# Optimization experiments

Hardware: AMD Instinct MI355X
Metric: run time of the kernel (lower is better)

Reference implementation:

```python
import jax, jax.numpy as jnp
import numpy as np

D_MODEL = 1024
H = 16
D_K = D_MODEL // H
D_FF = 4096
EPS = 1e-6
NEG = -1e9


def setup_inputs() -> dict:
    key = jax.random.key(0)
    ks = jax.random.split(key, 8)
    B, S = 2, 2048
    src = jax.random.normal(ks[0], (B, S, D_MODEL), dtype=jnp.float32)
    src_mask = jnp.ones((B, 1, 1, S), dtype=jnp.int32)
    sc = 1.0 / np.sqrt(D_MODEL)
    wq = jax.random.normal(ks[1], (D_MODEL, D_MODEL), jnp.float32) * sc
    wk = jax.random.normal(ks[2], (D_MODEL, D_MODEL), jnp.float32) * sc
    wv = jax.random.normal(ks[3], (D_MODEL, D_MODEL), jnp.float32) * sc
    wo = jax.random.normal(ks[4], (D_MODEL, D_MODEL), jnp.float32) * sc
    w1 = jax.random.normal(ks[5], (D_FF, D_MODEL), jnp.float32) * sc
    b1 = jnp.zeros((D_FF,), jnp.float32)
    w2 = jax.random.normal(ks[6], (D_MODEL, D_FF), jnp.float32) * (1.0 / np.sqrt(D_FF))
    b2 = jnp.zeros((D_MODEL,), jnp.float32)
    a1 = jnp.ones((1,), jnp.float32)
    be1 = jnp.zeros((1,), jnp.float32)
    a2 = jnp.ones((1,), jnp.float32)
    be2 = jnp.zeros((1,), jnp.float32)
    return dict(src=src, src_mask=src_mask, wq=wq, wk=wk, wv=wv, wo=wo,
                w1=w1, b1=b1, w2=w2, b2=b2, a1=a1, be1=be1, a2=a2, be2=be2)


def layer_norm(x, alpha, bias):
    # torch: mean + unbiased std (ddof=1), eps added to std
    mean = jnp.mean(x, axis=-1, keepdims=True)
    std = jnp.sqrt(jnp.var(x, axis=-1, keepdims=True, ddof=1))
    return alpha * (x - mean) / (std + EPS) + bias


def mha(x, mask, wq, wk, wv, wo):
    B, S, _ = x.shape
    def split(t):  # [B,S,D] -> [B,H,S,D_K]
        return t.reshape(B, S, H, D_K).transpose(0, 2, 1, 3)
    q = split(x @ wq.T)
    k = split(x @ wk.T)
    v = split(x @ wv.T)
    scores = jnp.einsum('bhqd,bhkd->bhqk', q, k) / np.sqrt(D_K)
    scores = jnp.where(mask == 0, NEG, scores)
    attn = jax.nn.softmax(scores, axis=-1)
    out = jnp.einsum('bhqk,bhkd->bhqd', attn, v)
    out = out.transpose(0, 2, 1, 3).reshape(B, S, D_MODEL)
    return out @ wo.T


def reference(src, src_mask, wq, wk, wv, wo, w1, b1, w2, b2, a1, be1, a2, be2):
    x = layer_norm(src, a1, be1)
    src = src + mha(x, src_mask, wq, wk, wv, wo)
    x = layer_norm(src, a2, be2)
    ff = jax.nn.relu(x @ w1.T + b1) @ w2.T + b2
    return src + ff
```

## Files before the change

kernel.cpp:

```cpp
#include <hip/hip_runtime.h>
#include <hip/hip_bf16.h>

typedef unsigned short u16;
typedef unsigned int u32;
typedef float floatx4 __attribute__((ext_vector_type(4)));
typedef __bf16 bf16x8 __attribute__((ext_vector_type(8)));
typedef u16 ushort4v __attribute__((ext_vector_type(4)));
typedef u16 ushort8v __attribute__((ext_vector_type(8)));

#define DEVI static __device__ __forceinline__

DEVI u16 f2bf(float f) {
    u32 u = __builtin_bit_cast(u32, f);
    u += 0x7fffu + ((u >> 16) & 1u);
    return (u16)(u >> 16);
}
DEVI float bf2f(u16 h) { return __builtin_bit_cast(float, (u32)h << 16); }

DEVI float fexp2(float x) { return __builtin_amdgcn_exp2f(x); }

DEVI void async_cp16(const u16* g, u16* l) {
    __builtin_amdgcn_global_load_lds((const __attribute__((address_space(1))) u32*)g,
                                     (__attribute__((address_space(3))) u32*)l, 16, 0, 0);
}

template<int BM, int BN, int RW, int CW, bool QKV3, int NSPLIT,
         bool BIAS, bool RELU, bool RESID, bool OBF16>
__global__ __launch_bounds__(256) void gemm_nt(
    const u16* __restrict__ A,
    const u16* __restrict__ W0, const u16* __restrict__ W1, const u16* __restrict__ W2,
    const float* __restrict__ bias, const float* __restrict__ resid,
    void* __restrict__ o0, void* __restrict__ o1, void* __restrict__ o2,
    void* __restrict__ o3, int K, int lda, int Nper, int NX)
{
    static_assert(RW * CW == 4, "4 waves");
    constexpr int WM = BM / RW, WN = BN / CW;
    constexpr int MI = WM / 16, NI = WN / 16;
    __shared__ __align__(16) u16 As[2][BM * 32];
    __shared__ __align__(16) u16 Bs[2][BN * 32];
    const int tid = threadIdx.x;
    const int w = tid >> 6, lane = tid & 63;
    const int q = lane >> 4, ml = lane & 15;
    const int wr = w / CW, wc = w % CW;
    const int m0 = blockIdx.y * BM;
    int bx = blockIdx.x;
    size_t kbase = 0;
    const u16* W = W0;
    void* outp = o0;
    if (NSPLIT > 1) {
        int part = bx / NX; bx -= part * NX; kbase = (size_t)part * K;
        outp = (part == 0) ? o0 : (part == 1 ? o1 : (part == 2 ? o2 : o3));
    }
    int n0 = bx * BN;
    if (QKV3) {
        int sel = n0 / Nper;
        n0 -= sel * Nper;
        W = (sel == 0) ? W0 : (sel == 1 ? W1 : W2);
        outp = (sel == 0) ? o0 : (sel == 1 ? o1 : o2);
    }

    auto stage = [&](int buf, int kt) {
#pragma unroll
        for (int p = 0; p < BM / 64; ++p) {
            int g = p * 256 + tid;
            int r = g >> 2, s = g & 3;
            int c = s ^ ((r >> 1) & 3);
            async_cp16(A + (size_t)(m0 + r) * lda + kbase + kt + c * 8,
                       &As[buf][(p * 256 + w * 64) * 8]);
        }
#pragma unroll
        for (int p = 0; p < BN / 64; ++p) {
            int g = p * 256 + tid;
            int r = g >> 2, s = g & 3;
            int c = s ^ ((r >> 1) & 3);
            async_cp16(W + (size_t)(n0 + r) * lda + kbase + kt + c * 8,
                       &Bs[buf][(p * 256 + w * 64) * 8]);
        }
    };

    const floatx4 fzero = {0.f, 0.f, 0.f, 0.f};
    floatx4 acc[MI][NI];
#pragma unroll
    for (int i = 0; i < MI; ++i)
#pragma unroll
        for (int j = 0; j < NI; ++j) acc[i][j] = fzero;

    stage(0, 0);
    for (int it = 0, kt = 0; kt < K; ++it, kt += 32) {
        __syncthreads();
        if (kt + 32 < K) stage((it + 1) & 1, kt + 32);
        const u16* Asb = As[it & 1];
        const u16* Bsb = Bs[it & 1];
        bf16x8 af[MI], bfr[NI];
#pragma unroll
        for (int i = 0; i < MI; ++i) {
            int rm = wr * WM + i * 16 + ml;
            int s = q ^ ((rm >> 1) & 3);
            af[i] = *(const bf16x8*)&Asb[(rm * 4 + s) * 8];
        }
#pragma unroll
        for (int j = 0; j < NI; ++j) {
            int rn = wc * WN + j * 16 + ml;
            int s = q ^ ((rn >> 1) & 3);
            bfr[j] = *(const bf16x8*)&Bsb[(rn * 4 + s) * 8];
        }
#pragma unroll
        for (int i = 0; i < MI; ++i)
#pragma unroll
            for (int j = 0; j < NI; ++j)
                acc[i][j] = __builtin_amdgcn_mfma_f32_16x16x32_bf16(af[i], bfr[j], acc[i][j], 0, 0, 0);
    }

#pragma unroll
    for (int j = 0; j < NI; ++j) {
        int gn = n0 + wc * WN + j * 16 + ml;
        float bj = 0.f;
        if (BIAS) bj = bias[gn];
#pragma unroll
        for (int i = 0; i < MI; ++i) {
            int gm0 = m0 + wr * WM + i * 16 + q * 4;
#pragma unroll
            for (int r = 0; r < 4; ++r) {
                size_t idx = (size_t)(gm0 + r) * Nper + gn;
                float v = acc[i][j][r] + bj;
                if (RELU) v = fmaxf(v, 0.f);
                if (RESID) v += resid[idx];
                if (OBF16) ((u16*)outp)[idx] = f2bf(v);
                else       ((float*)outp)[idx] = v;
            }
        }
    }
}

__global__ __launch_bounds__(128, 2) void flash7(
    const u16* __restrict__ Q, const u16* __restrict__ Kg,
    const u16* __restrict__ Vt, const float* __restrict__ biasv,
    u16* __restrict__ O)
{
    __shared__ __align__(16) u16 Ks[2][64 * 64];
    __shared__ __align__(16) u16 Vs[2][64 * 64];
    const int tid = threadIdx.x;
    const int w = tid >> 6, lane = tid & 63;
    const int q = lane >> 4, ml = lane & 15;
    const int b = blockIdx.y >> 4, h = blockIdx.y & 15;
    const size_t rowQ = (size_t)(b * 2048 + blockIdx.x * 64);
    const float KSC = 0.125f * 1.4426950408889634f;
    const floatx4 fzero = {0.f, 0.f, 0.f, 0.f};

    bf16x8 qa[2][2];
#pragma unroll
    for (int qg = 0; qg < 2; ++qg)
#pragma unroll
        for (int c = 0; c < 2; ++c)
            qa[qg][c] = *(const bf16x8*)&Q[(rowQ + w * 32 + qg * 16 + ml) * 1024
                                           + h * 64 + q * 8 + c * 32];

    auto stage = [&](int buf, int s0) {
#pragma unroll
        for (int p = 0; p < 4; ++p) {
            int L = p * 128 + tid;
            int row = L >> 3, sl = L & 7;
            int ch = sl ^ ((row & 3) | (((row >> 3) & 1) << 2));
            async_cp16(Kg + (size_t)(b * 2048 + s0 + row) * 1024 + h * 64 + ch * 8,
                       &Ks[buf][(p * 128 + w * 64) * 8]);
            async_cp16(Vt + (size_t)(b * 1024 + h * 64 + row) * 2048 + s0 + ch * 8,
                       &Vs[buf][(p * 128 + w * 64) * 8]);
        }
    };

    floatx4 oacc[2][4];
    float lsum[2] = {0.f, 0.f};
#pragma unroll
    for (int qg = 0; qg < 2; ++qg)
#pragma unroll
        for (int d = 0; d < 4; ++d) oacc[qg][d] = fzero;

    const int swk = (ml & 3) | (((ml >> 2) & 1) << 2);
    const int swv = (ml & 3) | (((ml >> 3) & 1) << 2);

    stage(0, 0);
    for (int it = 0; it < 32; ++it) {
        __syncthreads();
        if (it + 1 < 32) stage((it + 1) & 1, (it + 1) * 64);
        const u16* Kb = Ks[it & 1];
        const u16* Vb = Vs[it & 1];
        const int s0 = it * 64;

        bf16x8 pfrag[2][2];
#pragma unroll
        for (int g = 0; g < 2; ++g) {
            const int re = g * 32 + ((ml >> 2) << 3) + (ml & 3);
            bf16x8 ke0 = *(const bf16x8*)&Kb[(re + 0) * 64 + ((0 + q) ^ swk) * 8];
            bf16x8 ke1 = *(const bf16x8*)&Kb[(re + 0) * 64 + ((4 + q) ^ swk) * 8];
            bf16x8 ko0 = *(const bf16x8*)&Kb[(re + 4) * 64 + ((0 + q) ^ swk) * 8];
            bf16x8 ko1 = *(const bf16x8*)&Kb[(re + 4) * 64 + ((4 + q) ^ swk) * 8];
            const float4 be = *(const float4*)&biasv[b * 2048 + s0 + g * 32 + q * 8];
            const float4 bo = *(const float4*)&biasv[b * 2048 + s0 + g * 32 + q * 8 + 4];
#pragma unroll
            for (int qg = 0; qg < 2; ++qg) {
                floatx4 te = fzero, to = fzero;
                te = __builtin_amdgcn_mfma_f32_16x16x32_bf16(ke0, qa[qg][0], te, 0, 0, 0);
                te = __builtin_amdgcn_mfma_f32_16x16x32_bf16(ke1, qa[qg][1], te, 0, 0, 0);
                to = __builtin_amdgcn_mfma_f32_16x16x32_bf16(ko0, qa[qg][0], to, 0, 0, 0);
                to = __builtin_amdgcn_mfma_f32_16x16x32_bf16(ko1, qa[qg][1], to, 0, 0, 0);
                float pe0 = fexp2(fmaf(te[0], KSC, be.x));
                float pe1 = fexp2(fmaf(te[1], KSC, be.y));
                float pe2 = fexp2(fmaf(te[2], KSC, be.z));
                float pe3 = fexp2(fmaf(te[3], KSC, be.w));
                float po0 = fexp2(fmaf(to[0], KSC, bo.x));
                float po1 = fexp2(fmaf(to[1], KSC, bo.y));
                float po2 = fexp2(fmaf(to[2], KSC, bo.z));
                float po3 = fexp2(fmaf(to[3], KSC, bo.w));
                lsum[qg] += ((pe0 + pe1) + (pe2 + pe3)) + ((po0 + po1) + (po2 + po3));
                u32 pk[4];
                pk[0] = ((__builtin_bit_cast(u32, pe0) + 0x8000u) >> 16)
                      | ((__builtin_bit_cast(u32, pe1) + 0x8000u) & 0xffff0000u);
                pk[1] = ((__builtin_bit_cast(u32, pe2) + 0x8000u) >> 16)
                      | ((__builtin_bit_cast(u32, pe3) + 0x8000u) & 0xffff0000u);
                pk[2] = ((__builtin_bit_cast(u32, po0) + 0x8000u) >> 16)
                      | ((__builtin_bit_cast(u32, po1) + 0x8000u) & 0xffff0000u);
                pk[3] = ((__builtin_bit_cast(u32, po2) + 0x8000u) >> 16)
                      | ((__builtin_bit_cast(u32, po3) + 0x8000u) & 0xffff0000u);
                pfrag[g][qg] = __builtin_bit_cast(bf16x8, *(uint4*)pk);
            }
        }
#pragma unroll
        for (int dt = 0; dt < 4; ++dt) {
            int vrow = dt * 16 + ml;
#pragma unroll
            for (int g = 0; g < 2; ++g) {
                bf16x8 vf = *(const bf16x8*)&Vb[vrow * 64 + ((g * 4 + q) ^ swv) * 8];
#pragma unroll
                for (int qg = 0; qg < 2; ++qg)
                    oacc[qg][dt] = __builtin_amdgcn_mfma_f32_16x16x32_bf16(
                        vf, pfrag[g][qg], oacc[qg][dt], 0, 0, 0);
            }
        }
    }
#pragma unroll
    for (int qg = 0; qg < 2; ++qg) {
        float ls = lsum[qg];
        ls += __shfl_xor(ls, 16, 64);
        ls += __shfl_xor(ls, 32, 64);
        const float rcp = 1.f / ls;
        const size_t row = rowQ + w * 32 + qg * 16 + ml;
#pragma unroll
        for (int dt = 0; dt < 4; ++dt)
#pragma unroll
            for (int rp = 0; rp < 4; rp += 2) {
                u32 pk = (u32)f2bf(oacc[qg][dt][rp] * rcp)
                       | ((u32)f2bf(oacc[qg][dt][rp + 1] * rcp) << 16);
                *(u32*)&O[row * 1024 + h * 64 + dt * 16 + q * 4 + rp] = pk;
            }
    }
}

__global__ __launch_bounds__(256) void vtrans(const u16* __restrict__ Vb, u16* __restrict__ Vt)
{
    __shared__ __align__(16) u16 T[64 * 72];
    const int tid = threadIdx.x;
    const int ct = blockIdx.x, rt = blockIdx.y;
    const int b = rt >> 5;
    const int s0 = (rt & 31) * 64;
    const int c0 = ct * 64;
#pragma unroll
    for (int p = 0; p < 2; ++p) {
        int slot = p * 256 + tid;
        int lr = slot >> 3, pc = slot & 7;
        bf16x8 v = *(const bf16x8*)&Vb[(size_t)(b * 2048 + s0 + lr) * 1024 + c0 + pc * 8];
        *(bf16x8*)&T[lr * 72 + pc * 8] = v;
    }
    __syncthreads();
#pragma unroll
    for (int p = 0; p < 2; ++p) {
        int slot = p * 256 + tid;
        int dc = slot >> 3, sc0 = (slot & 7) * 8;
        ushort8v o;
#pragma unroll
        for (int j = 0; j < 8; ++j) o[j] = T[(sc0 + j) * 72 + dc];
        *(ushort8v*)&Vt[(size_t)(b * 1024 + c0 + dc) * 2048 + s0 + sc0] = o;
    }
}

DEVI void ln_row(const float* __restrict__ x, float ga, float gb,
                 u16* __restrict__ y, int row, int tid)
{
    const float4 v = ((const float4*)(x + (size_t)row * 1024))[tid];
    float s = v.x + v.y + v.z + v.w;
    float ss = v.x * v.x + v.y * v.y + v.z * v.z + v.w * v.w;
#pragma unroll
    for (int d = 1; d < 64; d <<= 1) { s += __shfl_xor(s, d, 64); ss += __shfl_xor(ss, d, 64); }
    __shared__ float ps[4], pss[4];
    const int w = tid >> 6, lane = tid & 63;
    if (lane == 0) { ps[w] = s; pss[w] = ss; }
    __syncthreads();
    s = ps[0] + ps[1] + ps[2] + ps[3];
    ss = pss[0] + pss[1] + pss[2] + pss[3];
    float mean = s * (1.f / 1024.f);
    float var = fmaxf((ss - s * mean) * (1.f / 1023.f), 0.f);
    float sc = ga / (sqrtf(var) + 1e-6f);
    ushort4v o;
    o[0] = f2bf((v.x - mean) * sc + gb);
    o[1] = f2bf((v.y - mean) * sc + gb);
    o[2] = f2bf((v.z - mean) * sc + gb);
    o[3] = f2bf((v.w - mean) * sc + gb);
    ((ushort4v*)(y + (size_t)row * 1024))[tid] = o;
}

__global__ __launch_bounds__(256) void ln_bf16(const float* __restrict__ x,
    const float* __restrict__ ga, const float* __restrict__ gb, u16* __restrict__ y)
{
    ln_row(x, ga[0], gb[0], y, blockIdx.x, threadIdx.x);
}

__global__ __launch_bounds__(256) void prep(
    const float* __restrict__ wq, const float* __restrict__ wk,
    const float* __restrict__ wv, const float* __restrict__ wo,
    const float* __restrict__ w1, const float* __restrict__ w2,
    u16* __restrict__ wqb, u16* __restrict__ wkb, u16* __restrict__ wvb,
    u16* __restrict__ wob, u16* __restrict__ w1b, u16* __restrict__ w2b,
    const int* __restrict__ m, float* __restrict__ biasv,
    const float* __restrict__ src, const float* __restrict__ a1,
    const float* __restrict__ be1, u16* __restrict__ xln1)
{
    const int bx = blockIdx.x;
    if (bx < 12288) {
        size_t i = (size_t)bx * 256 + threadIdx.x;
        const float* s; u16* d; size_t off;
        if (i < 262144)       { s = wq; d = wqb; off = i; }
        else if (i < 524288)  { s = wk; d = wkb; off = i - 262144; }
        else if (i < 786432)  { s = wv; d = wvb; off = i - 524288; }
        else if (i < 1048576) { s = wo; d = wob; off = i - 786432; }
        else if (i < 2097152) { s = w1; d = w1b; off = i - 1048576; }
        else                  { s = w2; d = w2b; off = i - 2097152; }
        float4 v = ((const float4*)s)[off];
        ushort4v o = {f2bf(v.x), f2bf(v.y), f2bf(v.z), f2bf(v.w)};
        ((ushort4v*)d)[off] = o;
    } else if (bx < 12304) {
        int i = (bx - 12288) * 256 + threadIdx.x;
        biasv[i] = m[i] ? 0.f : -1.442695e9f;
    } else {
        ln_row(src, a1[0], be1[0], xln1, bx - 12304, threadIdx.x);
    }
}

__global__ __launch_bounds__(256) void ff2_fin(
    const u16* __restrict__ p0, const u16* __restrict__ p1,
    const u16* __restrict__ p2, const u16* __restrict__ p3,
    const float* __restrict__ b2, const float* __restrict__ resid,
    float* __restrict__ out)
{
    const size_t i = (size_t)blockIdx.x * 256 + threadIdx.x;
    ushort4v a = *(const ushort4v*)&p0[i * 4];
    ushort4v b = *(const ushort4v*)&p1[i * 4];
    ushort4v c = *(const ushort4v*)&p2[i * 4];
    ushort4v d = *(const ushort4v*)&p3[i * 4];
    float4 r = ((const float4*)resid)[i];
    float4 bb = ((const float4*)b2)[i & 255];
    float4 o;
    o.x = (bf2f(a[0]) + bf2f(b[0])) + (bf2f(c[0]) + bf2f(d[0])) + r.x + bb.x;
    o.y = (bf2f(a[1]) + bf2f(b[1])) + (bf2f(c[1]) + bf2f(d[1])) + r.y + bb.y;
    o.z = (bf2f(a[2]) + bf2f(b[2])) + (bf2f(c[2]) + bf2f(d[2])) + r.z + bb.z;
    o.w = (bf2f(a[3]) + bf2f(b[3])) + (bf2f(c[3]) + bf2f(d[3])) + r.w + bb.w;
    ((float4*)out)[i] = o;
}

extern "C" void kernel_launch(void* const* d_in, const int* in_sizes, int n_in,
                              void* d_out, int out_size, void* d_ws, size_t ws_size,
                              hipStream_t stream)
{
    const float* src = (const float*)d_in[0];
    const int* msk   = (const int*)d_in[1];
    const float* wq  = (const float*)d_in[2];
    const float* wk  = (const float*)d_in[3];
    const float* wv  = (const float*)d_in[4];
    const float* wo  = (const float*)d_in[5];
    const float* w1  = (const float*)d_in[6];
    const float* b1  = (const float*)d_in[7];
    const float* w2  = (const float*)d_in[8];
    const float* b2  = (const float*)d_in[9];
    const float* a1  = (const float*)d_in[10];
    const float* be1 = (const float*)d_in[11];
    const float* a2  = (const float*)d_in[12];
    const float* be2 = (const float*)d_in[13];
    float* out = (float*)d_out;

    char* ws = (char*)d_ws;
    const size_t MB = (size_t)1 << 20;
    u16* wqb  = (u16*)(ws + 0 * MB);
    u16* wkb  = (u16*)(ws + 2 * MB);
    u16* wvb  = (u16*)(ws + 4 * MB);
    u16* wob  = (u16*)(ws + 6 * MB);
    u16* w1b  = (u16*)(ws + 8 * MB);
    u16* w2b  = (u16*)(ws + 16 * MB);
    u16* xln1 = (u16*)(ws + 24 * MB);
    u16* attn = xln1;
    u16* Qb   = (u16*)(ws + 32 * MB);
    u16* xln2 = Qb;
    u16* Kb   = (u16*)(ws + 40 * MB);
    u16* Vb   = (u16*)(ws + 48 * MB);
    u16* Vt   = (u16*)(ws + 56 * MB);
    float* biasv = (float*)(ws + 64 * MB);
    u16* h1   = (u16*)(ws + 40 * MB);
    float* src2 = (float*)(ws + 72 * MB);
    u16* P0 = (u16*)(ws + 0 * MB);
    u16* P1 = (u16*)(ws + 8 * MB);
    u16* P2 = (u16*)(ws + 24 * MB);
    u16* P3 = (u16*)(ws + 32 * MB);

    prep<<<16400, 256, 0, stream>>>(wq, wk, wv, wo, w1, w2,
                                    wqb, wkb, wvb, wob, w1b, w2b,
                                    msk, biasv, src, a1, be1, xln1);

    gemm_nt<128, 128, 2, 2, true, 1, false, false, false, true><<<dim3(24, 32), 256, 0, stream>>>(
        xln1, wqb, wkb, wvb, nullptr, nullptr, Qb, Kb, Vb, nullptr, 1024, 1024, 1024, 0);

    vtrans<<<dim3(16, 64), 256, 0, stream>>>(Vb, Vt);

    flash7<<<dim3(32, 32), 128, 0, stream>>>(Qb, Kb, Vt, biasv, attn);

    gemm_nt<128, 64, 4, 1, false, 1, false, false, true, false><<<dim3(16, 32), 256, 0, stream>>>(
        attn, wob, nullptr, nullptr, nullptr, src, src2, nullptr, nullptr, nullptr,
        1024, 1024, 1024, 0);

    ln_bf16<<<4096, 256, 0, stream>>>(src2, a2, be2, xln2);

    gemm_nt<128, 128, 2, 2, false, 1, true, true, false, true><<<dim3(32, 32), 256, 0, stream>>>(
        xln2, w1b, nullptr, nullptr, b1, nullptr, h1, nullptr, nullptr, nullptr,
        1024, 1024, 4096, 0);

    gemm_nt<128, 128, 2, 2, false, 4, false, false, false, true><<<dim3(32, 32), 256, 0, stream>>>(
        h1, w2b, nullptr, nullptr, nullptr, nullptr, P0, P1, P2, P3,
        1024, 4096, 1024, 8);

    ff2_fin<<<4096, 256, 0, stream>>>(P0, P1, P2, P3, b2, src2, out);
}
```

Before: 369.0 us.

## Add XCD-aware block swizzle to GEMMs and halve FF2 split-K factor

Adds an XSWZ template option that remaps the linear block id so that consecutive blocks sent to the same XCD (id mod 8) share M-row tiles. This is meant to improve L2 reuse of A tiles on the chiplet-partitioned MI355X. It is enabled for all four GEMMs. Separately, the FF2 GEMM split-K drops from 4 to 2 partitions (K=2048 each, 512 blocks instead of 1024), which cuts partial-sum traffic and simplifies the final reduction kernel but reduces parallelism. The swizzle assumes gridDim.y is divisible by 8.

```diff
diff --git a/kernel.cpp b/kernel.cpp
--- a/kernel.cpp
+++ b/kernel.cpp
@@ -24,7 +24,7 @@
                                      (__attribute__((address_space(3))) u32*)l, 16, 0, 0);
 }
 
-template<int BM, int BN, int RW, int CW, bool QKV3, int NSPLIT,
+template<int BM, int BN, int RW, int CW, bool QKV3, int NSPLIT, bool XSWZ,
          bool BIAS, bool RELU, bool RESID, bool OBF16>
 __global__ __launch_bounds__(256) void gemm_nt(
     const u16* __restrict__ A,
@@ -42,8 +42,16 @@
     const int w = tid >> 6, lane = tid & 63;
     const int q = lane >> 4, ml = lane & 15;
     const int wr = w / CW, wc = w % CW;
-    const int m0 = blockIdx.y * BM;
-    int bx = blockIdx.x;
+    int bx = blockIdx.x, by = blockIdx.y;
+    if (XSWZ) {
+        const int gx = gridDim.x, gy = gridDim.y;
+        int L = by * gx + bx;
+        int xcd = L & 7, s = L >> 3;
+        int mb = gy >> 3;
+        by = xcd * mb + s % mb;
+        bx = s / mb;
+    }
+    const int m0 = by * BM;
     size_t kbase = 0;
     const u16* W = W0;
     void* outp = o0;
@@ -346,22 +354,19 @@
 
 __global__ __launch_bounds__(256) void ff2_fin(
     const u16* __restrict__ p0, const u16* __restrict__ p1,
-    const u16* __restrict__ p2, const u16* __restrict__ p3,
     const float* __restrict__ b2, const float* __restrict__ resid,
     float* __restrict__ out)
 {
     const size_t i = (size_t)blockIdx.x * 256 + threadIdx.x;
     ushort4v a = *(const ushort4v*)&p0[i * 4];
     ushort4v b = *(const ushort4v*)&p1[i * 4];
-    ushort4v c = *(const ushort4v*)&p2[i * 4];
-    ushort4v d = *(const ushort4v*)&p3[i * 4];
     float4 r = ((const float4*)resid)[i];
     float4 bb = ((const float4*)b2)[i & 255];
     float4 o;
-    o.x = (bf2f(a[0]) + bf2f(b[0])) + (bf2f(c[0]) + bf2f(d[0])) + r.x + bb.x;
-    o.y = (bf2f(a[1]) + bf2f(b[1])) + (bf2f(c[1]) + bf2f(d[1])) + r.y + bb.y;
-    o.z = (bf2f(a[2]) + bf2f(b[2])) + (bf2f(c[2]) + bf2f(d[2])) + r.z + bb.z;
-    o.w = (bf2f(a[3]) + bf2f(b[3])) + (bf2f(c[3]) + bf2f(d[3])) + r.w + bb.w;
+    o.x = (bf2f(a[0]) + bf2f(b[0])) + r.x + bb.x;
+    o.y = (bf2f(a[1]) + bf2f(b[1])) + r.y + bb.y;
+    o.z = (bf2f(a[2]) + bf2f(b[2])) + r.z + bb.z;
+    o.w = (bf2f(a[3]) + bf2f(b[3])) + r.w + bb.w;
     ((float4*)out)[i] = o;
 }
 
@@ -404,34 +409,32 @@
     u16* h1   = (u16*)(ws + 40 * MB);
     float* src2 = (float*)(ws + 72 * MB);
     u16* P0 = (u16*)(ws + 0 * MB);
-    u16* P1 = (u16*)(ws + 8 * MB);
-    u16* P2 = (u16*)(ws + 24 * MB);
-    u16* P3 = (u16*)(ws + 32 * MB);
+    u16* P1 = (u16*)(ws + 24 * MB);
 
     prep<<<16400, 256, 0, stream>>>(wq, wk, wv, wo, w1, w2,
                                     wqb, wkb, wvb, wob, w1b, w2b,
                                     msk, biasv, src, a1, be1, xln1);
 
-    gemm_nt<128, 128, 2, 2, true, 1, false, false, false, true><<<dim3(24, 32), 256, 0, stream>>>(
+    gemm_nt<128, 128, 2, 2, true, 1, true, false, false, false, true><<<dim3(24, 32), 256, 0, stream>>>(
         xln1, wqb, wkb, wvb, nullptr, nullptr, Qb, Kb, Vb, nullptr, 1024, 1024, 1024, 0);
 
     vtrans<<<dim3(16, 64), 256, 0, stream>>>(Vb, Vt);
 
     flash7<<<dim3(32, 32), 128, 0, stream>>>(Qb, Kb, Vt, biasv, attn);
 
-    gemm_nt<128, 64, 4, 1, false, 1, false, false, true, false><<<dim3(16, 32), 256, 0, stream>>>(
+    gemm_nt<128, 64, 4, 1, false, 1, true, false, false, true, false><<<dim3(16, 32), 256, 0, stream>>>(
         attn, wob, nullptr, nullptr, nullptr, src, src2, nullptr, nullptr, nullptr,
         1024, 1024, 1024, 0);
 
     ln_bf16<<<4096, 256, 0, stream>>>(src2, a2, be2, xln2);
 
-    gemm_nt<128, 128, 2, 2, false, 1, true, true, false, true><<<dim3(32, 32), 256, 0, stream>>>(
+    gemm_nt<128, 128, 2, 2, false, 1, true, true, true, false, true><<<dim3(32, 32), 256, 0, stream>>>(
         xln2, w1b, nullptr, nullptr, b1, nullptr, h1, nullptr, nullptr, nullptr,
         1024, 1024, 4096, 0);
 
-    gemm_nt<128, 128, 2, 2, false, 4, false, false, false, true><<<dim3(32, 32), 256, 0, stream>>>(
-        h1, w2b, nullptr, nullptr, nullptr, nullptr, P0, P1, P2, P3,
-        1024, 4096, 1024, 8);
-
-    ff2_fin<<<4096, 256, 0, stream>>>(P0, P1, P2, P3, b2, src2, out);
-}
+    gemm_nt<128, 128, 2, 2, false, 2, true, false, false, false, true><<<dim3(16, 32), 256, 0, stream>>>(
+        h1, w2b, nullptr, nullptr, nullptr, nullptr, P0, P1, nullptr, nullptr,
+        2048, 4096, 1024, 8);
+
+    ff2_fin<<<4096, 256, 0, stream>>>(P0, P1, b2, src2, out);
+}
```

Result: faster. 356.3 us (-3.4%).
